# Optimization experiments

Measured on AMD Instinct MI355X. Metric: run time of the kernel, lower is better.

Reference implementation:

```python
import jax, jax.numpy as jnp
import numpy as np

N_NODES = 50000
N_EDGES = 800000
IN_DIM = 64
HEADS = 8
DHEAD = 8
CLAMP = 5.0


def _xavier(key, shape, fan_in, fan_out):
    std = jnp.sqrt(2.0 / (fan_in + fan_out))
    return std * jax.random.normal(key, shape, dtype=jnp.float32)


def setup_inputs() -> dict:
    key = jax.random.key(0)
    ks = jax.random.split(key, 12)
    HD = HEADS * DHEAD
    x = jax.random.normal(ks[0], (N_NODES, IN_DIM), dtype=jnp.float32)
    edge_attr = jax.random.normal(ks[1], (N_EDGES, IN_DIM), dtype=jnp.float32)
    edge_index = jax.random.randint(ks[2], (2, N_EDGES), 0, N_NODES, dtype=jnp.int32)
    # Linear weights stored as [in, out] so y = x @ W + b
    WQ = _xavier(ks[3], (IN_DIM, HD), IN_DIM, HD)
    bQ = jnp.zeros((HD,), jnp.float32)
    WK = _xavier(ks[4], (IN_DIM, HD), IN_DIM, HD)
    bK = jnp.zeros((HD,), jnp.float32)
    WE = _xavier(ks[5], (IN_DIM, 2 * HD), IN_DIM, 2 * HD)
    bE = jnp.zeros((2 * HD,), jnp.float32)
    WV = _xavier(ks[6], (IN_DIM, HD), IN_DIM, HD)
    bV = jnp.zeros((HD,), jnp.float32)
    Aw = _xavier(ks[7], (DHEAD, HEADS, 1), DHEAD * HEADS, 1)
    VeRow = _xavier(ks[8], (DHEAD, HEADS, DHEAD), DHEAD * HEADS, DHEAD)
    return {"x": x, "edge_attr": edge_attr, "edge_index": edge_index,
            "WQ": WQ, "bQ": bQ, "WK": WK, "bK": bK, "WE": WE, "bE": bE,
            "WV": WV, "bV": bV, "Aw": Aw, "VeRow": VeRow}


def _forward(x, edge_attr, edge_index, WQ, bQ, WK, bK, WE, bE, WV, bV, Aw, VeRow):
    N = x.shape[0]
    src_idx = edge_index[0]
    dst_idx = edge_index[1]
    Q_h = (x @ WQ + bQ).reshape(N, HEADS, DHEAD)
    K_h = (x @ WK + bK).reshape(N, HEADS, DHEAD)
    V_h = (x @ WV + bV).reshape(N, HEADS, DHEAD)
    E = (edge_attr @ WE + bE).reshape(-1, HEADS, 2 * DHEAD)  # [E,H,2D]
    E_w, E_b = E[:, :, :DHEAD], E[:, :, DHEAD:]
    # per-edge score: gather + signed-sqrt transform
    score = K_h[src_idx] + Q_h[dst_idx]              # [E,H,D]
    score = score * E_w
    score = jnp.sqrt(jax.nn.relu(score)) - jnp.sqrt(jax.nn.relu(-score))
    score = score + E_b                               # act = Identity
    e_t = score
    wE = score.reshape(score.shape[0], HEADS * DHEAD)
    # attention logits: contract over head dim with Aw -> [E,H,1]
    logit = jnp.einsum('ehd,dhc->ehc', score, Aw)
    logit = jnp.clip(logit, -CLAMP, CLAMP)
    # segment softmax over destination nodes (pyg_softmax)
    smax = jax.ops.segment_max(logit, dst_idx, num_segments=N)
    ex = jnp.exp(logit - smax[dst_idx])
    denom = jax.ops.segment_sum(ex, dst_idx, num_segments=N)[dst_idx] + 1e-16
    attn = ex / denom                                 # [E,H,1], dropout p=0
    # message passing: scatter-add weighted values
    msg = V_h[src_idx] * attn                         # [E,H,D]
    wV = jax.ops.segment_sum(msg, dst_idx, num_segments=N)
    # edge enhancement
    rowV = jax.ops.segment_sum(e_t * attn, dst_idx, num_segments=N)  # [N,H,D]
    wV = wV + jnp.einsum('nhd,dhc->nhc', rowV, VeRow)
    return wV, wE


def reference(x, edge_attr, edge_index, WQ, bQ, WK, bK, WE, bE, WV, bV, Aw, VeRow):
    return _forward(x, edge_attr, edge_index, WQ, bQ, WK, bK, WE, bE, WV, bV, Aw, VeRow)
```

## Files before the change

kernel.cpp:

```cpp
#include <hip/hip_runtime.h>
#include <hip/hip_bf16.h>
#include <math.h>

#define N_NODES 50000
#define N_EDGES 800000
#define CLAMP_V 5.0f

typedef short short8 __attribute__((ext_vector_type(8)));
typedef float f32x4  __attribute__((ext_vector_type(4)));

static __device__ inline short f2bf(float x) {
    __hip_bfloat16 h = __float2bfloat16(x);
    return __builtin_bit_cast(short, h);
}
static __device__ inline float bf2f(short s) {
    unsigned u = ((unsigned)(unsigned short)s) << 16;
    return __builtin_bit_cast(float, u);
}

__global__ __launch_bounds__(256) void qkv_kernel(
    const float* __restrict__ x,
    const float* __restrict__ WQ, const float* __restrict__ bQ,
    const float* __restrict__ WK, const float* __restrict__ bK,
    const float* __restrict__ WV, const float* __restrict__ bV,
    float* __restrict__ Q, float* __restrict__ K, float* __restrict__ V)
{
    const int t = threadIdx.x;
    const int c = t & 63;
    const int nl = t >> 6;
    const int base = blockIdx.x * 16;

    float accQ[4], accK[4], accV[4];
    int nodes[4];
#pragma unroll
    for (int j = 0; j < 4; ++j) {
        nodes[j] = base + j * 4 + nl;
        accQ[j] = bQ[c]; accK[j] = bK[c]; accV[j] = bV[c];
    }
    for (int k = 0; k < 64; ++k) {
        const float wq = WQ[k * 64 + c];
        const float wk = WK[k * 64 + c];
        const float wv = WV[k * 64 + c];
#pragma unroll
        for (int j = 0; j < 4; ++j) {
            const float xv = x[nodes[j] * 64 + k];
            accQ[j] += xv * wq;
            accK[j] += xv * wk;
            accV[j] += xv * wv;
        }
    }
#pragma unroll
    for (int j = 0; j < 4; ++j) {
        const int n = nodes[j];
        Q[n * 64 + c] = accQ[j];
        K[n * 64 + c] = accK[j];
        V[n * 64 + c] = accV[j];
    }
}

__global__ __launch_bounds__(256, 3) void edge_kernel(
    const float* __restrict__ edge_attr,
    const int* __restrict__ src_idx, const int* __restrict__ dst_idx,
    const float* __restrict__ WE, const float* __restrict__ bE,
    const float* __restrict__ Aw,
    const float* __restrict__ Qn, const float* __restrict__ Kn,
    const float* __restrict__ Vn, const float* __restrict__ VeRow,
    float* __restrict__ wE_out, float* __restrict__ denom,
    float* __restrict__ wV_num)
{
    __shared__ __align__(16) char raw[40960];
    __shared__ float bEs[128];
    __shared__ float Aws[64];
    __shared__ float VeL[512];

    short8* Bhi = (short8*)raw;
    short8* Blo = (short8*)(raw + 16384);

    const int t = threadIdx.x;
    const int wave = t >> 6;
    const int lane = t & 63;

    short* BhiE = (short*)raw;
    short* BloE = (short*)(raw + 16384);
    for (int i = t; i < 8192; i += 256) {
        const int j  = i & 7;
        const int ln = (i >> 3) & 63;
        const int kh = (i >> 9) & 1;
        const int ct = i >> 10;
        const int k   = kh * 32 + ((ln >> 4) << 3) + j;
        const int col = (ct << 4) + (ln & 15);
        const float w = WE[k * 128 + col];
        const short hb = f2bf(w);
        BhiE[i] = hb;
        BloE[i] = f2bf(w - bf2f(hb));
    }
    if (t < 128) bEs[t] = bE[t];
    if (t < 64)  Aws[t] = Aw[t];
    for (int i = t; i < 512; i += 256) VeL[i] = VeRow[i];
    __syncthreads();

    float* Ebuf_w = (float*)(raw + 32768 + wave * 2048);

    const int h    = lane >> 3;
    const int kk   = lane & 7;
    const int g    = lane >> 4;
    const int c4   = lane & 15;
    const int h16k = (h << 4) + kk;

    for (int it = blockIdx.x; it < 12500; it += gridDim.x) {
        const int ebase = __builtin_amdgcn_readfirstlane(it * 64 + wave * 16);

        int se[16], de[16];
#pragma unroll
        for (int r = 0; r < 16; ++r) {
            se[r] = src_idx[ebase + r];
            de[r] = dst_idx[ebase + r];
        }

        float4 au[2], av[2];
#pragma unroll
        for (int p = 0; p < 2; ++p) {
            const float* srcp = edge_attr + (size_t)(ebase + c4) * 64 + p * 32 + (g << 3);
            au[p] = *(const float4*)srcp;
            av[p] = *(const float4*)(srcp + 4);
        }

        float kv[16], qv[16], vv[16];
#pragma unroll
        for (int r = 0; r < 16; ++r) {
            kv[r] = Kn[se[r] * 64 + lane];
            qv[r] = Qn[de[r] * 64 + lane];
            vv[r] = Vn[se[r] * 64 + lane];
        }

        short8 ah[2], al[2];
#pragma unroll
        for (int p = 0; p < 2; ++p) {
            const float xv[8] = {au[p].x, au[p].y, au[p].z, au[p].w,
                                 av[p].x, av[p].y, av[p].z, av[p].w};
#pragma unroll
            for (int j = 0; j < 8; ++j) {
                const short hb = f2bf(xv[j]);
                ah[p][j] = hb;
                al[p][j] = f2bf(xv[j] - bf2f(hb));
            }
        }

        f32x4 acc[8] = {};
#pragma unroll
        for (int kh = 0; kh < 2; ++kh) {
#pragma unroll
            for (int ct = 0; ct < 8; ++ct) {
                const short8 bh = Bhi[(ct * 2 + kh) * 64 + lane];
                const short8 bl = Blo[(ct * 2 + kh) * 64 + lane];
                acc[ct] = __builtin_amdgcn_mfma_f32_16x16x32_bf16(ah[kh], bh, acc[ct], 0, 0, 0);
                acc[ct] = __builtin_amdgcn_mfma_f32_16x16x32_bf16(al[kh], bh, acc[ct], 0, 0, 0);
                acc[ct] = __builtin_amdgcn_mfma_f32_16x16x32_bf16(ah[kh], bl, acc[ct], 0, 0, 0);
            }
        }

#pragma unroll
        for (int q = 0; q < 4; ++q) {
            if (g == q) {
#pragma unroll
                for (int ct = 0; ct < 8; ++ct) {
                    const int col = (ct << 4) + c4;
                    const float b = bEs[col];
                    f32x4 vq = acc[ct];
                    vq[0] += b; vq[1] += b; vq[2] += b; vq[3] += b;
                    *(f32x4*)(Ebuf_w + col * 4) = vq;
                }
            }
            __asm__ volatile("s_waitcnt lgkmcnt(0)" ::: "memory");
            __builtin_amdgcn_sched_barrier(0);
#pragma unroll
            for (int rr = 0; rr < 4; ++rr) {
                const int e = ebase + q * 4 + rr;
                const int d = de[q * 4 + rr];
                const float kq = kv[q * 4 + rr] + qv[q * 4 + rr];
                const float ew = Ebuf_w[h16k * 4 + rr];
                const float eb = Ebuf_w[(h16k + 8) * 4 + rr];
                float sc = kq * ew;
                sc = copysignf(sqrtf(fabsf(sc)), sc) + eb;
                wE_out[(size_t)e * 64 + lane] = sc;

                float pp = sc * Aws[kk * 8 + h];
                pp += __shfl_xor(pp, 1);
                pp += __shfl_xor(pp, 2);
                pp += __shfl_xor(pp, 4);
                pp = fminf(fmaxf(pp, -CLAMP_V), CLAMP_V);
                const float ex = __expf(pp);
                if (kk == 0) unsafeAtomicAdd(&denom[d * 8 + h], ex);

                float rsum = 0.f;
#pragma unroll
                for (int dd = 0; dd < 8; ++dd) {
                    const float etd = __shfl(sc, (lane & 56) + dd);
                    rsum += etd * VeL[dd * 64 + lane];
                }
                unsafeAtomicAdd(&wV_num[(size_t)d * 64 + lane],
                                ex * (vv[q * 4 + rr] + rsum));
            }
            __builtin_amdgcn_sched_barrier(0);
        }
    }
}

__global__ __launch_bounds__(256) void finalize_kernel(
    const float* __restrict__ denom, float* __restrict__ wV)
{
    const int i = blockIdx.x * 256 + threadIdx.x;
    const int n = i >> 6;
    const int h = (i >> 3) & 7;
    const float dn = denom[n * 8 + h] + 1e-16f;
    wV[i] = wV[i] / dn;
}

extern "C" void kernel_launch(void* const* d_in, const int* in_sizes, int n_in,
                              void* d_out, int out_size, void* d_ws, size_t ws_size,
                              hipStream_t stream) {
    const float* x         = (const float*)d_in[0];
    const float* edge_attr = (const float*)d_in[1];
    const int*   ei        = (const int*)  d_in[2];
    const float* WQ = (const float*)d_in[3];
    const float* bQ = (const float*)d_in[4];
    const float* WK = (const float*)d_in[5];
    const float* bK = (const float*)d_in[6];
    const float* WE = (const float*)d_in[7];
    const float* bE = (const float*)d_in[8];
    const float* WV = (const float*)d_in[9];
    const float* bV = (const float*)d_in[10];
    const float* Aw = (const float*)d_in[11];
    const float* VeRow = (const float*)d_in[12];

    float* out    = (float*)d_out;
    float* wV_out = out;
    float* wE_out = out + (size_t)N_NODES * 64;

    float* ws    = (float*)d_ws;
    float* Q     = ws;
    float* K     = ws + 3200000;
    float* V     = ws + 6400000;
    float* denom = ws + 9600000;

    const int* src_idx = ei;
    const int* dst_idx = ei + N_EDGES;

    hipMemsetAsync(wV_out, 0, (size_t)N_NODES * 64 * sizeof(float), stream);
    hipMemsetAsync(denom, 0, (size_t)N_NODES * 8 * sizeof(float), stream);

    qkv_kernel<<<3125, 256, 0, stream>>>(x, WQ, bQ, WK, bK, WV, bV, Q, K, V);
    edge_kernel<<<768, 256, 0, stream>>>(edge_attr, src_idx, dst_idx, WE, bE, Aw,
                                         Q, K, V, VeRow, wE_out, denom, wV_out);
    finalize_kernel<<<12500, 256, 0, stream>>>(denom, wV_out);
}
```

Baseline: 335.7 us.

## Software-pipeline edge loop: prefetch next tile's indices, attrs, Q/K gathers

Restructures the persistent edge loop into a two-stage software pipeline with ping-pong register sets. While the current tile runs its MFMAs and atomics, the next tile's edge indices, edge_attr rows and K/Q gathers are issued and its bf16 split is prepared, to hide gather latency. Aw and VeRow now sit in registers rather than LDS. This raises register pressure under launch_bounds(256,3), which may cause spills or lower occupancy.

```diff
diff --git a/kernel.cpp b/kernel.cpp
--- a/kernel.cpp
+++ b/kernel.cpp
@@ -70,8 +70,6 @@
 {
     __shared__ __align__(16) char raw[40960];
     __shared__ float bEs[128];
-    __shared__ float Aws[64];
-    __shared__ float VeL[512];
 
     short8* Bhi = (short8*)raw;
     short8* Blo = (short8*)(raw + 16384);
@@ -95,8 +93,6 @@
         BloE[i] = f2bf(w - bf2f(hb));
     }
     if (t < 128) bEs[t] = bE[t];
-    if (t < 64)  Aws[t] = Aw[t];
-    for (int i = t; i < 512; i += 256) VeL[i] = VeRow[i];
     __syncthreads();
 
     float* Ebuf_w = (float*)(raw + 32768 + wave * 2048);
@@ -107,43 +103,41 @@
     const int c4   = lane & 15;
     const int h16k = (h << 4) + kk;
 
-    for (int it = blockIdx.x; it < 12500; it += gridDim.x) {
-        const int ebase = __builtin_amdgcn_readfirstlane(it * 64 + wave * 16);
-
-        int se[16], de[16];
+    const float aw = Aw[kk * 8 + h];
+    float veR[8];
+#pragma unroll
+    for (int dd = 0; dd < 8; ++dd) veR[dd] = VeRow[dd * 64 + lane];
+
+    int se0[16], de0[16], se1[16], de1[16];
+    float kv0[16], qv0[16], kv1[16], qv1[16];
+    float4 ar0[4], ar1[4];
+    short8 ah0[2], al0[2], ah1[2], al1[2];
+
+    const int G = (int)gridDim.x;
+
+    auto body = [&](int (&seC)[16], int (&deC)[16], float (&kvC)[16], float (&qvC)[16],
+                    short8 (&ahC)[2], short8 (&alC)[2],
+                    int (&seN)[16], int (&deN)[16], float (&kvN)[16], float (&qvN)[16],
+                    float4 (&arN)[4], short8 (&ahN)[2], short8 (&alN)[2],
+                    int itC, int itN) {
+        const int ebaseC = __builtin_amdgcn_readfirstlane(itC * 64 + wave * 16);
+        const int itNc   = (itN < 12500) ? itN : 0;
+        const int ebaseN = __builtin_amdgcn_readfirstlane(itNc * 64 + wave * 16);
+
+        float vvC[16];
+#pragma unroll
+        for (int r = 0; r < 16; ++r) vvC[r] = Vn[seC[r] * 64 + lane];
+
+#pragma unroll
+        for (int p = 0; p < 2; ++p) {
+            const float* srcp = edge_attr + (size_t)(ebaseN + c4) * 64 + p * 32 + (g << 3);
+            arN[2 * p]     = *(const float4*)srcp;
+            arN[2 * p + 1] = *(const float4*)(srcp + 4);
+        }
 #pragma unroll
         for (int r = 0; r < 16; ++r) {
-            se[r] = src_idx[ebase + r];
-            de[r] = dst_idx[ebase + r];
-        }
-
-        float4 au[2], av[2];
-#pragma unroll
-        for (int p = 0; p < 2; ++p) {
-            const float* srcp = edge_attr + (size_t)(ebase + c4) * 64 + p * 32 + (g << 3);
-            au[p] = *(const float4*)srcp;
-            av[p] = *(const float4*)(srcp + 4);
-        }
-
-        float kv[16], qv[16], vv[16];
-#pragma unroll
-        for (int r = 0; r < 16; ++r) {
-            kv[r] = Kn[se[r] * 64 + lane];
-            qv[r] = Qn[de[r] * 64 + lane];
-            vv[r] = Vn[se[r] * 64 + lane];
-        }
-
-        short8 ah[2], al[2];
-#pragma unroll
-        for (int p = 0; p < 2; ++p) {
-            const float xv[8] = {au[p].x, au[p].y, au[p].z, au[p].w,
-                                 av[p].x, av[p].y, av[p].z, av[p].w};
-#pragma unroll
-            for (int j = 0; j < 8; ++j) {
-                const short hb = f2bf(xv[j]);
-                ah[p][j] = hb;
-                al[p][j] = f2bf(xv[j] - bf2f(hb));
-            }
+            seN[r] = src_idx[ebaseN + r];
+            deN[r] = dst_idx[ebaseN + r];
         }
 
         f32x4 acc[8] = {};
@@ -153,10 +147,16 @@
             for (int ct = 0; ct < 8; ++ct) {
                 const short8 bh = Bhi[(ct * 2 + kh) * 64 + lane];
                 const short8 bl = Blo[(ct * 2 + kh) * 64 + lane];
-                acc[ct] = __builtin_amdgcn_mfma_f32_16x16x32_bf16(ah[kh], bh, acc[ct], 0, 0, 0);
-                acc[ct] = __builtin_amdgcn_mfma_f32_16x16x32_bf16(al[kh], bh, acc[ct], 0, 0, 0);
-                acc[ct] = __builtin_amdgcn_mfma_f32_16x16x32_bf16(ah[kh], bl, acc[ct], 0, 0, 0);
-            }
+                acc[ct] = __builtin_amdgcn_mfma_f32_16x16x32_bf16(ahC[kh], bh, acc[ct], 0, 0, 0);
+                acc[ct] = __builtin_amdgcn_mfma_f32_16x16x32_bf16(alC[kh], bh, acc[ct], 0, 0, 0);
+                acc[ct] = __builtin_amdgcn_mfma_f32_16x16x32_bf16(ahC[kh], bl, acc[ct], 0, 0, 0);
+            }
+        }
+
+#pragma unroll
+        for (int r = 0; r < 16; ++r) {
+            kvN[r] = Kn[seN[r] * 64 + lane];
+            qvN[r] = Qn[deN[r] * 64 + lane];
         }
 
 #pragma unroll
@@ -175,16 +175,16 @@
             __builtin_amdgcn_sched_barrier(0);
 #pragma unroll
             for (int rr = 0; rr < 4; ++rr) {
-                const int e = ebase + q * 4 + rr;
-                const int d = de[q * 4 + rr];
-                const float kq = kv[q * 4 + rr] + qv[q * 4 + rr];
+                const int e = ebaseC + q * 4 + rr;
+                const int d = deC[q * 4 + rr];
+                const float kq = kvC[q * 4 + rr] + qvC[q * 4 + rr];
                 const float ew = Ebuf_w[h16k * 4 + rr];
                 const float eb = Ebuf_w[(h16k + 8) * 4 + rr];
                 float sc = kq * ew;
                 sc = copysignf(sqrtf(fabsf(sc)), sc) + eb;
                 wE_out[(size_t)e * 64 + lane] = sc;
 
-                float pp = sc * Aws[kk * 8 + h];
+                float pp = sc * aw;
                 pp += __shfl_xor(pp, 1);
                 pp += __shfl_xor(pp, 2);
                 pp += __shfl_xor(pp, 4);
@@ -196,13 +196,70 @@
 #pragma unroll
                 for (int dd = 0; dd < 8; ++dd) {
                     const float etd = __shfl(sc, (lane & 56) + dd);
-                    rsum += etd * VeL[dd * 64 + lane];
+                    rsum += etd * veR[dd];
                 }
                 unsafeAtomicAdd(&wV_num[(size_t)d * 64 + lane],
-                                ex * (vv[q * 4 + rr] + rsum));
+                                ex * (vvC[q * 4 + rr] + rsum));
             }
             __builtin_amdgcn_sched_barrier(0);
         }
+
+#pragma unroll
+        for (int p = 0; p < 2; ++p) {
+            const float xv[8] = {arN[2*p].x, arN[2*p].y, arN[2*p].z, arN[2*p].w,
+                                 arN[2*p+1].x, arN[2*p+1].y, arN[2*p+1].z, arN[2*p+1].w};
+#pragma unroll
+            for (int j = 0; j < 8; ++j) {
+                const short hb = f2bf(xv[j]);
+                ahN[p][j] = hb;
+                alN[p][j] = f2bf(xv[j] - bf2f(hb));
+            }
+        }
+    };
+
+    int it = blockIdx.x;
+    {
+        const int ebase0 = __builtin_amdgcn_readfirstlane(it * 64 + wave * 16);
+#pragma unroll
+        for (int p = 0; p < 2; ++p) {
+            const float* srcp = edge_attr + (size_t)(ebase0 + c4) * 64 + p * 32 + (g << 3);
+            ar0[2 * p]     = *(const float4*)srcp;
+            ar0[2 * p + 1] = *(const float4*)(srcp + 4);
+        }
+#pragma unroll
+        for (int r = 0; r < 16; ++r) {
+            se0[r] = src_idx[ebase0 + r];
+            de0[r] = dst_idx[ebase0 + r];
+        }
+#pragma unroll
+        for (int r = 0; r < 16; ++r) {
+            kv0[r] = Kn[se0[r] * 64 + lane];
+            qv0[r] = Qn[de0[r] * 64 + lane];
+        }
+#pragma unroll
+        for (int p = 0; p < 2; ++p) {
+            const float xv[8] = {ar0[2*p].x, ar0[2*p].y, ar0[2*p].z, ar0[2*p].w,
+                                 ar0[2*p+1].x, ar0[2*p+1].y, ar0[2*p+1].z, ar0[2*p+1].w};
+#pragma unroll
+            for (int j = 0; j < 8; ++j) {
+                const short hb = f2bf(xv[j]);
+                ah0[p][j] = hb;
+                al0[p][j] = f2bf(xv[j] - bf2f(hb));
+            }
+        }
+    }
+
+    while (true) {
+        int itN = it + G;
+        body(se0, de0, kv0, qv0, ah0, al0,
+             se1, de1, kv1, qv1, ar1, ah1, al1, it, itN);
+        it = itN;
+        if (it >= 12500) break;
+        itN = it + G;
+        body(se1, de1, kv1, qv1, ah1, al1,
+             se0, de0, kv0, qv0, ar0, ah0, al0, it, itN);
+        it = itN;
+        if (it >= 12500) break;
     }
 }
 
```

New measurement: 498.7 us. +48.6%, slower.

## Software-pipeline edge_attr and index loads; keep Aw/VeRow in registers

Applied to the files above, without the earlier changes.

Prefetches the next iteration's edge_attr rows and src/dst indices into registers while the current edge tile runs its MFMA and scatter phase, so global load latency overlaps with compute. It also moves the per-lane Aw coefficient and VeRow column from shared memory into registers, removing LDS reads from the inner loop. In exchange, register pressure rises (a second set of 16 src and 16 dst indices plus four float4s), which could lower occupancy under the launch_bounds(256,3) constraint or cause spills.

```diff
diff --git a/kernel.cpp b/kernel.cpp
--- a/kernel.cpp
+++ b/kernel.cpp
@@ -70,8 +70,6 @@
 {
     __shared__ __align__(16) char raw[40960];
     __shared__ float bEs[128];
-    __shared__ float Aws[64];
-    __shared__ float VeL[512];
 
     short8* Bhi = (short8*)raw;
     short8* Blo = (short8*)(raw + 16384);
@@ -95,8 +93,6 @@
         BloE[i] = f2bf(w - bf2f(hb));
     }
     if (t < 128) bEs[t] = bE[t];
-    if (t < 64)  Aws[t] = Aw[t];
-    for (int i = t; i < 512; i += 256) VeL[i] = VeRow[i];
     __syncthreads();
 
     float* Ebuf_w = (float*)(raw + 32768 + wave * 2048);
@@ -107,43 +103,71 @@
     const int c4   = lane & 15;
     const int h16k = (h << 4) + kk;
 
-    for (int it = blockIdx.x; it < 12500; it += gridDim.x) {
-        const int ebase = __builtin_amdgcn_readfirstlane(it * 64 + wave * 16);
-
-        int se[16], de[16];
+    const float aw = Aw[kk * 8 + h];
+    float veR[8];
+#pragma unroll
+    for (int dd = 0; dd < 8; ++dd) veR[dd] = VeRow[dd * 64 + lane];
+
+    const int G = (int)gridDim.x;
+
+    float4 arC[4], arN[4];
+    int seC[16], deC[16], seN[16], deN[16];
+
+    int it = blockIdx.x;
+    {
+        const int ebase0 = __builtin_amdgcn_readfirstlane(it * 64 + wave * 16);
+#pragma unroll
+        for (int p = 0; p < 2; ++p) {
+            const float* srcp = edge_attr + (size_t)(ebase0 + c4) * 64 + p * 32 + (g << 3);
+            arC[2 * p]     = *(const float4*)srcp;
+            arC[2 * p + 1] = *(const float4*)(srcp + 4);
+        }
 #pragma unroll
         for (int r = 0; r < 16; ++r) {
-            se[r] = src_idx[ebase + r];
-            de[r] = dst_idx[ebase + r];
-        }
-
-        float4 au[2], av[2];
+            seC[r] = src_idx[ebase0 + r];
+            deC[r] = dst_idx[ebase0 + r];
+        }
+    }
+
+    for (; it < 12500; it += G) {
+        const int ebaseC = __builtin_amdgcn_readfirstlane(it * 64 + wave * 16);
+        const int itN    = it + G;
+        const int itNc   = (itN < 12500) ? itN : 0;
+        const int ebaseN = __builtin_amdgcn_readfirstlane(itNc * 64 + wave * 16);
+
+        short8 ah[2], al[2];
 #pragma unroll
         for (int p = 0; p < 2; ++p) {
-            const float* srcp = edge_attr + (size_t)(ebase + c4) * 64 + p * 32 + (g << 3);
-            au[p] = *(const float4*)srcp;
-            av[p] = *(const float4*)(srcp + 4);
-        }
-
-        float kv[16], qv[16], vv[16];
-#pragma unroll
-        for (int r = 0; r < 16; ++r) {
-            kv[r] = Kn[se[r] * 64 + lane];
-            qv[r] = Qn[de[r] * 64 + lane];
-            vv[r] = Vn[se[r] * 64 + lane];
-        }
-
-        short8 ah[2], al[2];
-#pragma unroll
-        for (int p = 0; p < 2; ++p) {
-            const float xv[8] = {au[p].x, au[p].y, au[p].z, au[p].w,
-                                 av[p].x, av[p].y, av[p].z, av[p].w};
+            const float xv[8] = {arC[2*p].x, arC[2*p].y, arC[2*p].z, arC[2*p].w,
+                                 arC[2*p+1].x, arC[2*p+1].y, arC[2*p+1].z, arC[2*p+1].w};
 #pragma unroll
             for (int j = 0; j < 8; ++j) {
                 const short hb = f2bf(xv[j]);
                 ah[p][j] = hb;
                 al[p][j] = f2bf(xv[j] - bf2f(hb));
             }
+        }
+
+#pragma unroll
+        for (int r = 0; r < 16; ++r) {
+            seN[r] = src_idx[ebaseN + r];
+            deN[r] = dst_idx[ebaseN + r];
+        }
+
+        float vv[16], kv[16], qv[16];
+#pragma unroll
+        for (int r = 0; r < 16; ++r) vv[r] = Vn[seC[r] * 64 + lane];
+#pragma unroll
+        for (int r = 0; r < 16; ++r) {
+            kv[r] = Kn[seC[r] * 64 + lane];
+            qv[r] = Qn[deC[r] * 64 + lane];
+        }
+
+#pragma unroll
+        for (int p = 0; p < 2; ++p) {
+            const float* srcp = edge_attr + (size_t)(ebaseN + c4) * 64 + p * 32 + (g << 3);
+            arN[2 * p]     = *(const float4*)srcp;
+            arN[2 * p + 1] = *(const float4*)(srcp + 4);
         }
 
         f32x4 acc[8] = {};
@@ -175,8 +199,8 @@
             __builtin_amdgcn_sched_barrier(0);
 #pragma unroll
             for (int rr = 0; rr < 4; ++rr) {
-                const int e = ebase + q * 4 + rr;
-                const int d = de[q * 4 + rr];
+                const int e = ebaseC + q * 4 + rr;
+                const int d = deC[q * 4 + rr];
                 const float kq = kv[q * 4 + rr] + qv[q * 4 + rr];
                 const float ew = Ebuf_w[h16k * 4 + rr];
                 const float eb = Ebuf_w[(h16k + 8) * 4 + rr];
@@ -184,7 +208,7 @@
                 sc = copysignf(sqrtf(fabsf(sc)), sc) + eb;
                 wE_out[(size_t)e * 64 + lane] = sc;
 
-                float pp = sc * Aws[kk * 8 + h];
+                float pp = sc * aw;
                 pp += __shfl_xor(pp, 1);
                 pp += __shfl_xor(pp, 2);
                 pp += __shfl_xor(pp, 4);
@@ -196,13 +220,18 @@
 #pragma unroll
                 for (int dd = 0; dd < 8; ++dd) {
                     const float etd = __shfl(sc, (lane & 56) + dd);
-                    rsum += etd * VeL[dd * 64 + lane];
+                    rsum += etd * veR[dd];
                 }
                 unsafeAtomicAdd(&wV_num[(size_t)d * 64 + lane],
                                 ex * (vv[q * 4 + rr] + rsum));
             }
             __builtin_amdgcn_sched_barrier(0);
         }
+
+#pragma unroll
+        for (int p = 0; p < 4; ++p) arC[p] = arN[p];
+#pragma unroll
+        for (int r = 0; r < 16; ++r) { seC[r] = seN[r]; deC[r] = deN[r]; }
     }
 }
 
```

Measured after the change: 326.6 us. -2.7%, faster.
